# Kernel optimization log

Hardware: AMD Instinct MI355X
Metric: run time of the kernel (lower is better)

## Reference

```python
import jax, jax.numpy as jnp
import numpy as np
import math

B, T, D = 2, 2048, 1024
H = 16
HD = D // H
DFF = 4096
EPS = 1e-5


def setup_inputs() -> dict:
    key = jax.random.key(0)
    ks = jax.random.split(key, 11)
    s = 0.02
    return {
        "x": jax.random.normal(ks[0], (B, T, D), dtype=jnp.float32),
        "scale1": jnp.ones((D,), jnp.float32),
        "scale2": jnp.ones((D,), jnp.float32),
        "Wqkv": jax.random.normal(ks[1], (D, 3 * D), jnp.float32) * s,
        "bqkv": jnp.zeros((3 * D,), jnp.float32),
        "Wo": jax.random.normal(ks[2], (D, D), jnp.float32) * s,
        "bo": jnp.zeros((D,), jnp.float32),
        "W1": jax.random.normal(ks[3], (D, DFF), jnp.float32) * s,
        "b1": jnp.zeros((DFF,), jnp.float32),
        "W2": jax.random.normal(ks[4], (DFF, D), jnp.float32) * s,
        "b2": jnp.zeros((D,), jnp.float32),
    }


def rmsnorm(x, scale):
    # Faithful to source: norm = ||x||/sqrt(d); out = scale * x / (norm + eps)
    d = x.shape[-1]
    norm = jnp.linalg.norm(x, axis=-1, keepdims=True) * (1.0 / math.sqrt(d))
    return scale * x / (norm + EPS)


def attention(x, Wqkv, bqkv, Wo, bo):
    b, t, c = x.shape
    qkv = x @ Wqkv + bqkv                       # [B,T,3D]
    qkv = qkv.reshape(b, t, 3, H, HD)
    q, k, v = qkv[:, :, 0], qkv[:, :, 1], qkv[:, :, 2]   # [B,T,H,HD]
    scores = jnp.einsum("bqhd,bkhd->bhqk", q, k) / math.sqrt(HD)
    w = jax.nn.softmax(scores, axis=-1)
    out = jnp.einsum("bhqk,bkhd->bqhd", w, v).reshape(b, t, c)
    return out @ Wo + bo


def reference(x, scale1, scale2, Wqkv, bqkv, Wo, bo, W1, b1, W2, b2):
    x = x + attention(rmsnorm(x, scale1), Wqkv, bqkv, Wo, bo)
    h = rmsnorm(x, scale2)
    ff = (jax.nn.gelu(h @ W1 + b1, approximate=False)) @ W2 + b2
    return x + ff
```

## Files before the change

kernel.cpp:

```cpp
#include <hip/hip_runtime.h>
#include <hip/hip_bf16.h>
#include <math.h>

typedef unsigned short u16;
typedef __bf16 bf16x8 __attribute__((ext_vector_type(8)));
typedef float f32x4 __attribute__((ext_vector_type(4)));
typedef unsigned int u32x2 __attribute__((ext_vector_type(2)));

#define B_   2
#define T_   2048
#define D_   1024
#define H_   16
#define HD_  64
#define DFF_ 4096
#define M_TOK (B_*T_)

__device__ __forceinline__ u16 f2bf(float f){
  unsigned u = __float_as_uint(f);
  u += 0x7fff + ((u>>16)&1);
  return (u16)(u>>16);
}

__device__ __forceinline__ void gl2lds16(const void* g, void* l){
  __builtin_amdgcn_global_load_lds((const __attribute__((address_space(1))) void*)g,
                                   (__attribute__((address_space(3))) void*)l, 16, 0, 0);
}

__device__ __forceinline__ unsigned lds_u32(const void* p){
  return (unsigned)(uintptr_t)(const __attribute__((address_space(3))) void*)p;
}

__device__ __forceinline__ u32x2 tr_read(unsigned addr){
  u32x2 d;
  asm volatile("ds_read_b64_tr_b16 %0, %1" : "=v"(d) : "v"(addr));
  return d;
}
__device__ __forceinline__ u32x2 tr_read512(unsigned addr){
  u32x2 d;
  asm volatile("ds_read_b64_tr_b16 %0, %1 offset:512" : "=v"(d) : "v"(addr));
  return d;
}
__device__ __forceinline__ bf16x8 pack8(u32x2 a, u32x2 b){
  union { u32x2 u[2]; bf16x8 v; } x; x.u[0]=a; x.u[1]=b; return x.v;
}

__global__ __launch_bounds__(256) void k_transpose_bf16(const float* __restrict__ in,
                                                        u16* __restrict__ out, int K, int N){
  __shared__ float t[32][33];
  int bx = blockIdx.x*32, by = blockIdx.y*32;
  int tx = threadIdx.x, ty = threadIdx.y;
  #pragma unroll
  for(int i=ty;i<32;i+=8) t[i][tx] = in[(size_t)(by+i)*N + bx + tx];
  __syncthreads();
  #pragma unroll
  for(int i=ty;i<32;i+=8) out[(size_t)(bx+i)*K + by + tx] = f2bf(t[tx][i]);
}

__global__ __launch_bounds__(256) void k_rmsnorm_bf16(const float* __restrict__ x,
                                                      const float* __restrict__ scale,
                                                      u16* __restrict__ out){
  int row = blockIdx.x;
  int tid = threadIdx.x;
  int lane = tid&63, wave = tid>>6;
  const float4* xr = (const float4*)(x + (size_t)row*D_);
  float4 v = xr[tid];
  float ss = v.x*v.x + v.y*v.y + v.z*v.z + v.w*v.w;
  #pragma unroll
  for(int o=1;o<64;o<<=1) ss += __shfl_xor(ss, o);
  __shared__ float red[4];
  if(lane==0) red[wave]=ss;
  __syncthreads();
  float tot = red[0]+red[1]+red[2]+red[3];
  float inv = 1.0f/(sqrtf(tot*(1.0f/D_)) + 1e-5f);
  const float4* sr = (const float4*)scale;
  float4 s4 = sr[tid];
  u16* o4 = out + (size_t)row*D_ + tid*4;
  o4[0]=f2bf(v.x*s4.x*inv); o4[1]=f2bf(v.y*s4.y*inv);
  o4[2]=f2bf(v.z*s4.z*inv); o4[3]=f2bf(v.w*s4.w*inv);
}

template<int EPI>
__global__ __launch_bounds__(256) void k_gemm(const u16* __restrict__ A, const u16* __restrict__ Bt,
                                              const float* __restrict__ bias, const float* __restrict__ res,
                                              void* __restrict__ Cout, int M, int N, int K){
  __shared__ u16 As[128*32];
  __shared__ u16 Bs[128*32];
  int tid = threadIdx.x;
  int lane = tid&63, wave = tid>>6;
  int wr = wave>>1, wc = wave&1;
  int row0 = blockIdx.x*128, col0 = blockIdx.y*128;
  f32x4 acc[4][4];
  #pragma unroll
  for(int m=0;m<4;m++)
    #pragma unroll
    for(int n=0;n<4;n++) acc[m][n] = (f32x4){0.f,0.f,0.f,0.f};
  const u16* Ag = A + (size_t)row0*K;
  const u16* Bg = Bt + (size_t)col0*K;
  for(int k0=0;k0<K;k0+=32){
    __syncthreads();
    #pragma unroll
    for(int c=tid;c<512;c+=256){
      gl2lds16(Ag + (size_t)(c>>2)*K + k0 + (c&3)*8, (char*)As + c*16);
      gl2lds16(Bg + (size_t)(c>>2)*K + k0 + (c&3)*8, (char*)Bs + c*16);
    }
    __syncthreads();
    const u16* ab = As + (wr*64 + (lane&15))*32 + (lane>>4)*8;
    const u16* bb = Bs + (wc*64 + (lane&15))*32 + (lane>>4)*8;
    bf16x8 a[4], b[4];
    #pragma unroll
    for(int m=0;m<4;m++) a[m] = *(const bf16x8*)(ab + m*16*32);
    #pragma unroll
    for(int n=0;n<4;n++) b[n] = *(const bf16x8*)(bb + n*16*32);
    #pragma unroll
    for(int m=0;m<4;m++)
      #pragma unroll
      for(int n=0;n<4;n++)
        acc[m][n] = __builtin_amdgcn_mfma_f32_16x16x32_bf16(a[m], b[n], acc[m][n], 0,0,0);
  }
  #pragma unroll
  for(int m=0;m<4;m++){
    #pragma unroll
    for(int n=0;n<4;n++){
      #pragma unroll
      for(int r=0;r<4;r++){
        int row = row0 + wr*64 + m*16 + (lane>>4)*4 + r;
        int col = col0 + wc*64 + n*16 + (lane&15);
        float v = acc[m][n][r] + bias[col];
        if constexpr(EPI==1){
          ((float*)Cout)[(size_t)row*N + col] = v + res[(size_t)row*N + col];
        } else if constexpr(EPI==2){
          v = 0.5f*v*(1.0f + erff(v*0.70710678118f));
          ((u16*)Cout)[(size_t)row*N + col] = f2bf(v);
        } else {
          ((u16*)Cout)[(size_t)row*N + col] = f2bf(v);
        }
      }
    }
  }
}

__global__ __launch_bounds__(256) void k_gemm_pk(const u16* __restrict__ A, const u16* __restrict__ Bt,
                                                 float* __restrict__ P, int M, int N, int K){
  __shared__ u16 As[128*32];
  __shared__ u16 Bs[128*32];
  int tid = threadIdx.x;
  int lane = tid&63, wave = tid>>6;
  int wr = wave>>1, wc = wave&1;
  int row0 = blockIdx.x*128, col0 = blockIdx.y*128;
  int kc = blockIdx.z;
  int klen = K/2, kbeg = kc*klen;
  f32x4 acc[4][4];
  #pragma unroll
  for(int m=0;m<4;m++)
    #pragma unroll
    for(int n=0;n<4;n++) acc[m][n] = (f32x4){0.f,0.f,0.f,0.f};
  const u16* Ag = A + (size_t)row0*K + kbeg;
  const u16* Bg = Bt + (size_t)col0*K + kbeg;
  for(int k0=0;k0<klen;k0+=32){
    __syncthreads();
    #pragma unroll
    for(int c=tid;c<512;c+=256){
      gl2lds16(Ag + (size_t)(c>>2)*K + k0 + (c&3)*8, (char*)As + c*16);
      gl2lds16(Bg + (size_t)(c>>2)*K + k0 + (c&3)*8, (char*)Bs + c*16);
    }
    __syncthreads();
    const u16* ab = As + (wr*64 + (lane&15))*32 + (lane>>4)*8;
    const u16* bb = Bs + (wc*64 + (lane&15))*32 + (lane>>4)*8;
    bf16x8 a[4], b[4];
    #pragma unroll
    for(int m=0;m<4;m++) a[m] = *(const bf16x8*)(ab + m*16*32);
    #pragma unroll
    for(int n=0;n<4;n++) b[n] = *(const bf16x8*)(bb + n*16*32);
    #pragma unroll
    for(int m=0;m<4;m++)
      #pragma unroll
      for(int n=0;n<4;n++)
        acc[m][n] = __builtin_amdgcn_mfma_f32_16x16x32_bf16(a[m], b[n], acc[m][n], 0,0,0);
  }
  float* Pk = P + (size_t)kc*M*N;
  #pragma unroll
  for(int m=0;m<4;m++)
    #pragma unroll
    for(int n=0;n<4;n++)
      #pragma unroll
      for(int r=0;r<4;r++){
        int row = row0 + wr*64 + m*16 + (lane>>4)*4 + r;
        int col = col0 + wc*64 + n*16 + (lane&15);
        Pk[(size_t)row*N + col] = acc[m][n][r];
      }
}

__global__ __launch_bounds__(256) void k_ff2_reduce(const float* __restrict__ P,
                                                    const float* __restrict__ bias,
                                                    const float* __restrict__ res,
                                                    float* __restrict__ out){
  const size_t total4 = (size_t)M_TOK*D_/4;
  const float4* p0 = (const float4*)P;
  const float4* p1 = (const float4*)(P + (size_t)M_TOK*D_);
  const float4* rr = (const float4*)res;
  const float4* bb = (const float4*)bias;
  float4* oo = (float4*)out;
  for(size_t i = (size_t)blockIdx.x*256 + threadIdx.x; i < total4; i += (size_t)gridDim.x*256){
    float4 a = p0[i], b = p1[i], r = rr[i], c = bb[i & (D_/4 - 1)];
    float4 o;
    o.x = (a.x+b.x)+(c.x+r.x);
    o.y = (a.y+b.y)+(c.y+r.y);
    o.z = (a.z+b.z)+(c.z+r.z);
    o.w = (a.w+b.w)+(c.w+r.w);
    oo[i] = o;
  }
}

__global__ __launch_bounds__(256,4) void k_attn(const u16* __restrict__ qkv, u16* __restrict__ O){
  __shared__ alignas(16) u16 Ks[2][4096];
  __shared__ alignas(16) u16 Vs[2][4096];
  __shared__ alignas(16) u16 Ps[4][1024];
  const int qt = blockIdx.x, h = blockIdx.y, b = blockIdx.z;
  const int tid = threadIdx.x, lane = tid&63, wave = tid>>6;
  const int lo = lane&15, hi = lane>>4, l7 = lane&7;
  const u16* qkvB = qkv + (size_t)b*T_*3072;
  const int hoff = h*64;

  const int q0 = qt*64 + wave*16;
  const u16* qp = qkvB + (size_t)(q0+lo)*3072 + hoff + hi*8;
  bf16x8 aq0 = *(const bf16x8*)qp;
  bf16x8 aq1 = *(const bf16x8*)(qp+32);

  size_t sK[2], sV[2];
  {
    int cc[2] = {tid, tid+256};
    #pragma unroll
    for(int i=0;i<2;i++){
      int c = cc[i];
      sK[i] = (size_t)(c>>3)*3072 + 1024 + hoff + (((c&7)^((c>>3)&7))<<3);
      int kv = ((c>>5)<<2) + ((c>>1)&3);
      int d0 = (((c&31)>>3)<<4) | ((c&1)<<3);
      sV[i] = (size_t)kv*3072 + 2048 + hoff + d0;
    }
  }
  const unsigned kb0 = (unsigned)lo*128 + (unsigned)((hi^l7))*16;
  const unsigned kb1 = (unsigned)lo*128 + (unsigned)(((hi|4)^l7))*16;
  const unsigned vtr = (unsigned)hi*1024 + (unsigned)lo*2;

  f32x4 oac[4];
  #pragma unroll
  for(int n=0;n<4;n++) oac[n] = (f32x4){0.f,0.f,0.f,0.f};
  float mrow[4] = {-1e30f,-1e30f,-1e30f,-1e30f};
  float lrow[4] = {0.f,0.f,0.f,0.f};

  {
    char* kd = (char*)Ks[0]; char* vd = (char*)Vs[0];
    gl2lds16(qkvB + sK[0], kd + tid*16);
    gl2lds16(qkvB + sK[1], kd + tid*16 + 4096);
    gl2lds16(qkvB + sV[0], vd + tid*16);
    gl2lds16(qkvB + sV[1], vd + tid*16 + 4096);
  }
  int buf = 0;
  for(int t=0;t<T_/64;t++){
    __syncthreads();
    if(t < T_/64-1){
      size_t koff = (size_t)(t+1)*64*3072;
      char* kd = (char*)Ks[buf^1]; char* vd = (char*)Vs[buf^1];
      gl2lds16(qkvB + koff + sK[0], kd + tid*16);
      gl2lds16(qkvB + koff + sK[1], kd + tid*16 + 4096);
      gl2lds16(qkvB + koff + sV[0], vd + tid*16);
      gl2lds16(qkvB + koff + sV[1], vd + tid*16 + 4096);
    }
    const char* K_ = (const char*)Ks[buf];
    u16* P_ = Ps[wave];

    f32x4 s[4];
    __builtin_amdgcn_s_setprio(1);
    #pragma unroll
    for(int n=0;n<4;n++){
      bf16x8 b0 = *(const bf16x8*)(K_ + n*2048 + kb0);
      bf16x8 b1 = *(const bf16x8*)(K_ + n*2048 + kb1);
      f32x4 z = (f32x4){0.f,0.f,0.f,0.f};
      z = __builtin_amdgcn_mfma_f32_16x16x32_bf16(aq0, b0, z, 0,0,0);
      z = __builtin_amdgcn_mfma_f32_16x16x32_bf16(aq1, b1, z, 0,0,0);
      s[n] = z;
    }
    __builtin_amdgcn_s_setprio(0);

    float mx[4]; int ok = 1;
    #pragma unroll
    for(int r=0;r<4;r++){
      mx[r] = fmaxf(fmaxf(s[0][r],s[1][r]),fmaxf(s[2][r],s[3][r]));
      ok &= (mx[r] <= mrow[r] + 64.0f) ? 1 : 0;
    }
    if(!__all(ok)){
      #pragma unroll
      for(int r=0;r<4;r++){
        float mm = mx[r];
        mm = fmaxf(mm, __shfl_xor(mm,1));
        mm = fmaxf(mm, __shfl_xor(mm,2));
        mm = fmaxf(mm, __shfl_xor(mm,4));
        mm = fmaxf(mm, __shfl_xor(mm,8));
        float nm = fmaxf(mrow[r], mm);
        float alpha = __expf((mrow[r]-nm)*0.125f);
        mrow[r] = nm;
        lrow[r] *= alpha;
        #pragma unroll
        for(int n=0;n<4;n++) oac[n][r] *= alpha;
      }
    }
    #pragma unroll
    for(int r=0;r<4;r++){
      float p[4];
      #pragma unroll
      for(int n=0;n<4;n++) p[n] = __expf((s[n][r]-mrow[r])*0.125f);
      lrow[r] += (p[0]+p[1])+(p[2]+p[3]);
      const int q = hi*4 + r;
      const unsigned X = (unsigned)(q&7)<<4;
      char* pb = (char*)P_ + q*128;
      #pragma unroll
      for(int n=0;n<4;n++)
        *(u16*)(pb + (((unsigned)(lo*2 + n*32))^X)) = f2bf(p[n]);
    }

    const unsigned vsb = lds_u32(Vs[buf]);
    #pragma unroll
    for(int kk=0;kk<2;kk++){
      bf16x8 ap = *(const bf16x8*)((const char*)P_ + (kk==0 ? kb0 : kb1));
      u32x2 t0[4], t1[4];
      #pragma unroll
      for(int n=0;n<4;n++){
        unsigned a = vsb + vtr + (unsigned)kk*4096 + (unsigned)n*128;
        t0[n] = tr_read(a);
        t1[n] = tr_read512(a);
      }
      asm volatile("s_waitcnt lgkmcnt(0)" ::: "memory");
      __builtin_amdgcn_sched_barrier(0);
      __builtin_amdgcn_s_setprio(1);
      #pragma unroll
      for(int n=0;n<4;n++){
        bf16x8 bv = pack8(t0[n], t1[n]);
        oac[n] = __builtin_amdgcn_mfma_f32_16x16x32_bf16(ap, bv, oac[n], 0,0,0);
      }
      __builtin_amdgcn_s_setprio(0);
    }
    buf ^= 1;
  }

  #pragma unroll
  for(int r=0;r<4;r++){
    float lr = lrow[r];
    lr += __shfl_xor(lr,1);
    lr += __shfl_xor(lr,2);
    lr += __shfl_xor(lr,4);
    lr += __shfl_xor(lr,8);
    lrow[r] = 1.0f/lr;
  }
  size_t obase = ((size_t)b*T_ + q0)*D_ + hoff;
  #pragma unroll
  for(int n=0;n<4;n++)
    #pragma unroll
    for(int r=0;r<4;r++)
      O[obase + (size_t)(hi*4+r)*D_ + n*16 + lo] = f2bf(oac[n][r]*lrow[r]);
}

extern "C" void kernel_launch(void* const* d_in, const int* in_sizes, int n_in,
                              void* d_out, int out_size, void* d_ws, size_t ws_size,
                              hipStream_t stream){
  (void)in_sizes; (void)n_in; (void)out_size; (void)ws_size;
  const float* x      = (const float*)d_in[0];
  const float* scale1 = (const float*)d_in[1];
  const float* scale2 = (const float*)d_in[2];
  const float* Wqkv   = (const float*)d_in[3];
  const float* bqkv   = (const float*)d_in[4];
  const float* Wo     = (const float*)d_in[5];
  const float* bo     = (const float*)d_in[6];
  const float* W1     = (const float*)d_in[7];
  const float* b1     = (const float*)d_in[8];
  const float* W2     = (const float*)d_in[9];
  const float* b2     = (const float*)d_in[10];
  float* out = (float*)d_out;

  char* w = (char*)d_ws;
  u16* xn1   = (u16*)w;  w += (size_t)M_TOK*D_*2;
  u16* qkvb  = (u16*)w;  w += (size_t)M_TOK*3*D_*2;
  u16* Obuf  = (u16*)w;  w += (size_t)M_TOK*D_*2;
  float* x2  = (float*)w; w += (size_t)M_TOK*D_*4;
  u16* xn2   = (u16*)w;  w += (size_t)M_TOK*D_*2;
  u16* h1    = (u16*)w;  w += (size_t)M_TOK*DFF_*2;
  u16* Wqkvt = (u16*)w;  w += (size_t)3*D_*D_*2;
  u16* Wot   = (u16*)w;  w += (size_t)D_*D_*2;
  u16* W1t   = (u16*)w;  w += (size_t)D_*DFF_*2;
  u16* W2t   = (u16*)w;  w += (size_t)DFF_*D_*2;
  float* pk  = (float*)d_ws;

  dim3 tb(32,8);
  k_transpose_bf16<<<dim3(3*D_/32, D_/32), tb, 0, stream>>>(Wqkv, Wqkvt, D_, 3*D_);
  k_transpose_bf16<<<dim3(D_/32,   D_/32), tb, 0, stream>>>(Wo,   Wot,   D_, D_);
  k_transpose_bf16<<<dim3(DFF_/32, D_/32), tb, 0, stream>>>(W1,   W1t,   D_, DFF_);
  k_transpose_bf16<<<dim3(D_/32, DFF_/32), tb, 0, stream>>>(W2,   W2t,   DFF_, D_);

  k_rmsnorm_bf16<<<M_TOK, 256, 0, stream>>>(x, scale1, xn1);
  k_gemm<0><<<dim3(M_TOK/128, 3*D_/128), 256, 0, stream>>>(xn1, Wqkvt, bqkv, nullptr, qkvb, M_TOK, 3*D_, D_);
  k_attn<<<dim3(T_/64, H_, B_), 256, 0, stream>>>(qkvb, Obuf);
  k_gemm<1><<<dim3(M_TOK/128, D_/128), 256, 0, stream>>>(Obuf, Wot, bo, x, x2, M_TOK, D_, D_);
  k_rmsnorm_bf16<<<M_TOK, 256, 0, stream>>>(x2, scale2, xn2);
  k_gemm<2><<<dim3(M_TOK/128, DFF_/128), 256, 0, stream>>>(xn2, W1t, b1, nullptr, h1, M_TOK, DFF_, D_);
  k_gemm_pk<<<dim3(M_TOK/128, D_/128, 2), 256, 0, stream>>>(h1, W2t, pk, M_TOK, D_, DFF_);
  k_ff2_reduce<<<2048, 256, 0, stream>>>(pk, b2, x2, out);
}
```

Before: 285.4 us.

## Transpose QK^T MFMA so each lane owns one query row in attention softmax

```diff
diff --git a/kernel.cpp b/kernel.cpp
--- a/kernel.cpp
+++ b/kernel.cpp
@@ -42,6 +42,11 @@
 }
 __device__ __forceinline__ bf16x8 pack8(u32x2 a, u32x2 b){
   union { u32x2 u[2]; bf16x8 v; } x; x.u[0]=a; x.u[1]=b; return x.v;
+}
+__device__ __forceinline__ unsigned cvt_pk_bf16(float a, float b){
+  unsigned r;
+  asm("v_cvt_pk_bf16_f32 %0, %1, %2" : "=v"(r) : "v"(a), "v"(b));
+  return r;
 }
 
 __global__ __launch_bounds__(256) void k_transpose_bf16(const float* __restrict__ in,
@@ -220,6 +225,7 @@
   const int lo = lane&15, hi = lane>>4, l7 = lane&7;
   const u16* qkvB = qkv + (size_t)b*T_*3072;
   const int hoff = h*64;
+  const float C2 = 0.18033688f;
 
   const int q0 = qt*64 + wave*16;
   const u16* qp = qkvB + (size_t)(q0+lo)*3072 + hoff + hi*8;
@@ -241,12 +247,13 @@
   const unsigned kb0 = (unsigned)lo*128 + (unsigned)((hi^l7))*16;
   const unsigned kb1 = (unsigned)lo*128 + (unsigned)(((hi|4)^l7))*16;
   const unsigned vtr = (unsigned)hi*1024 + (unsigned)lo*2;
+  const unsigned swzQ = (unsigned)(lo&7)<<4;
 
   f32x4 oac[4];
   #pragma unroll
   for(int n=0;n<4;n++) oac[n] = (f32x4){0.f,0.f,0.f,0.f};
-  float mrow[4] = {-1e30f,-1e30f,-1e30f,-1e30f};
-  float lrow[4] = {0.f,0.f,0.f,0.f};
+  float mrow = -1e30f;
+  float lsum = 0.f;
 
   {
     char* kd = (char*)Ks[0]; char* vd = (char*)Vs[0];
@@ -273,49 +280,49 @@
     __builtin_amdgcn_s_setprio(1);
     #pragma unroll
     for(int n=0;n<4;n++){
-      bf16x8 b0 = *(const bf16x8*)(K_ + n*2048 + kb0);
-      bf16x8 b1 = *(const bf16x8*)(K_ + n*2048 + kb1);
+      bf16x8 k0f = *(const bf16x8*)(K_ + n*2048 + kb0);
+      bf16x8 k1f = *(const bf16x8*)(K_ + n*2048 + kb1);
       f32x4 z = (f32x4){0.f,0.f,0.f,0.f};
-      z = __builtin_amdgcn_mfma_f32_16x16x32_bf16(aq0, b0, z, 0,0,0);
-      z = __builtin_amdgcn_mfma_f32_16x16x32_bf16(aq1, b1, z, 0,0,0);
+      z = __builtin_amdgcn_mfma_f32_16x16x32_bf16(k0f, aq0, z, 0,0,0);
+      z = __builtin_amdgcn_mfma_f32_16x16x32_bf16(k1f, aq1, z, 0,0,0);
       s[n] = z;
     }
     __builtin_amdgcn_s_setprio(0);
 
-    float mx[4]; int ok = 1;
-    #pragma unroll
-    for(int r=0;r<4;r++){
-      mx[r] = fmaxf(fmaxf(s[0][r],s[1][r]),fmaxf(s[2][r],s[3][r]));
-      ok &= (mx[r] <= mrow[r] + 64.0f) ? 1 : 0;
-    }
-    if(!__all(ok)){
-      #pragma unroll
-      for(int r=0;r<4;r++){
-        float mm = mx[r];
-        mm = fmaxf(mm, __shfl_xor(mm,1));
-        mm = fmaxf(mm, __shfl_xor(mm,2));
-        mm = fmaxf(mm, __shfl_xor(mm,4));
-        mm = fmaxf(mm, __shfl_xor(mm,8));
-        float nm = fmaxf(mrow[r], mm);
-        float alpha = __expf((mrow[r]-nm)*0.125f);
-        mrow[r] = nm;
-        lrow[r] *= alpha;
+    float mx = s[0][0];
+    #pragma unroll
+    for(int n=0;n<4;n++)
+      #pragma unroll
+      for(int r=0;r<4;r++) mx = fmaxf(mx, s[n][r]);
+
+    if(!__all(mx <= mrow + 64.0f)){
+      float mm = fmaxf(mx, __shfl_xor(mx,16));
+      mm = fmaxf(mm, __shfl_xor(mm,32));
+      float nm = fmaxf(mrow, mm);
+      float alpha = exp2f((mrow - nm)*C2);
+      mrow = nm;
+      lsum *= alpha;
+      float ar[4];
+      #pragma unroll
+      for(int r=0;r<4;r++) ar[r] = __shfl(alpha, hi*4 + r);
+      #pragma unroll
+      for(int n=0;n<4;n++)
         #pragma unroll
-        for(int n=0;n<4;n++) oac[n][r] *= alpha;
-      }
-    }
-    #pragma unroll
-    for(int r=0;r<4;r++){
-      float p[4];
-      #pragma unroll
-      for(int n=0;n<4;n++) p[n] = __expf((s[n][r]-mrow[r])*0.125f);
-      lrow[r] += (p[0]+p[1])+(p[2]+p[3]);
-      const int q = hi*4 + r;
-      const unsigned X = (unsigned)(q&7)<<4;
-      char* pb = (char*)P_ + q*128;
-      #pragma unroll
-      for(int n=0;n<4;n++)
-        *(u16*)(pb + (((unsigned)(lo*2 + n*32))^X)) = f2bf(p[n]);
+        for(int r=0;r<4;r++) oac[n][r] *= ar[r];
+    }
+
+    const float nmC2 = -mrow*C2;
+    #pragma unroll
+    for(int n=0;n<4;n++){
+      float p0v = exp2f(fmaf(s[n][0], C2, nmC2));
+      float p1v = exp2f(fmaf(s[n][1], C2, nmC2));
+      float p2v = exp2f(fmaf(s[n][2], C2, nmC2));
+      float p3v = exp2f(fmaf(s[n][3], C2, nmC2));
+      lsum += (p0v+p1v)+(p2v+p3v);
+      u32x2 pw;
+      pw[0] = cvt_pk_bf16(p0v, p1v);
+      pw[1] = cvt_pk_bf16(p2v, p3v);
+      *(u32x2*)((char*)P_ + (unsigned)lo*128 + (((unsigned)(n*32 + hi*8)) ^ swzQ)) = pw;
     }
 
     const unsigned vsb = lds_u32(Vs[buf]);
@@ -342,21 +349,18 @@
     buf ^= 1;
   }
 
-  #pragma unroll
-  for(int r=0;r<4;r++){
-    float lr = lrow[r];
-    lr += __shfl_xor(lr,1);
-    lr += __shfl_xor(lr,2);
-    lr += __shfl_xor(lr,4);
-    lr += __shfl_xor(lr,8);
-    lrow[r] = 1.0f/lr;
-  }
+  lsum += __shfl_xor(lsum, 16);
+  lsum += __shfl_xor(lsum, 32);
+  float linv = 1.0f/lsum;
+  float lr[4];
+  #pragma unroll
+  for(int r=0;r<4;r++) lr[r] = __shfl(linv, hi*4 + r);
   size_t obase = ((size_t)b*T_ + q0)*D_ + hoff;
   #pragma unroll
   for(int n=0;n<4;n++)
     #pragma unroll
     for(int r=0;r<4;r++)
-      O[obase + (size_t)(hi*4+r)*D_ + n*16 + lo] = f2bf(oac[n][r]*lrow[r]);
+      O[obase + (size_t)(hi*4+r)*D_ + n*16 + lo] = f2bf(oac[n][r]*lr[r]);
 }
 
 extern "C" void kernel_launch(void* const* d_in, const int* in_sizes, int n_in,
```

Measured after the change: 284.1 us. Within noise of the previous version (-0.5%).
